# Kernel tuning notes

Measured on AMD Instinct MI355X. Metric: run time of the kernel, lower is better.

The kernel has to match this reference:

```python
import jax, jax.numpy as jnp
import numpy as np

MASK_VALUE = 0.0
LEAKY_SLOPE = 0.2  # tf.keras 'leaky_relu' activation default negative_slope

B, T, F, H, OUT = 256, 512, 256, 1024, 64


def setup_inputs() -> dict:
    key = jax.random.key(0)
    ks = jax.random.split(key, 5)
    x = jax.random.normal(ks[0], (B, T, F), dtype=jnp.float32)
    W = jax.random.normal(ks[1], (F, 4 * H), dtype=jnp.float32) * 0.05
    U = jax.random.normal(ks[2], (H, 4 * H), dtype=jnp.float32) * 0.05
    b = jnp.zeros((4 * H,), dtype=jnp.float32)
    W1 = jax.random.normal(ks[3], (3 * H, H), dtype=jnp.float32) * 0.02
    b1 = jnp.zeros((H,), dtype=jnp.float32)
    W2 = jax.random.normal(ks[4], (H, OUT), dtype=jnp.float32) * 0.02
    b2 = jnp.zeros((OUT,), dtype=jnp.float32)
    return {"x": x, "W": W, "U": U, "b": b, "W1": W1, "b1": b1, "W2": W2, "b2": b2}


def _lstm_final_state(x, mask, W, U, b):
    """Masked LSTM (Keras gate order i,f,g,o); masked steps carry state through.
    Returns final (h, c), each [B, H]. Dropout layers are identity at inference."""
    h0 = jnp.zeros((x.shape[0], H), dtype=x.dtype)
    c0 = jnp.zeros((x.shape[0], H), dtype=x.dtype)
    # Precompute input projection for all timesteps in one big GEMM: [B,T,4H]
    xz = jnp.einsum('btf,fg->btg', x, W) + b

    def step(carry, inp):
        h, c = carry
        xz_t, m_t = inp  # [B,4H], [B]
        z = xz_t + h @ U
        i, f, g, o = jnp.split(z, 4, axis=-1)
        i = jax.nn.sigmoid(i)
        f = jax.nn.sigmoid(f)
        g = jnp.tanh(g)
        o = jax.nn.sigmoid(o)
        c_new = f * c + i * g
        h_new = o * jnp.tanh(c_new)
        m = m_t[:, None]
        h = jnp.where(m, h_new, h)
        c = jnp.where(m, c_new, c)
        return (h, c), None

    xs = (jnp.swapaxes(xz, 0, 1), jnp.swapaxes(mask, 0, 1))  # time-major
    (h, c), _ = jax.lax.scan(step, (h0, c0), xs)
    return h, c


def reference(x, W, U, b, W1, b1, W2, b2):
    mask = jnp.any(x != MASK_VALUE, axis=2)  # [B,T]
    h, c = _lstm_final_state(x, mask, W, U, b)
    # return_state=True with return_sequences=False -> (out, h, c), out == h
    feat = jnp.concatenate([h, h, c], axis=1)  # [B, 3H]
    y = jax.nn.leaky_relu(feat @ W1 + b1, negative_slope=LEAKY_SLOPE)
    return y @ W2 + b2
```

## Files before the change

### kernel.cpp

```cpp
#include <hip/hip_runtime.h>

#define Tt_ 512
#define Ff_ 256
#define Hh_ 1024

typedef unsigned short u16;
typedef unsigned long long u64;
typedef __attribute__((ext_vector_type(8))) short bf16x8;
typedef __attribute__((ext_vector_type(4))) float f32x4;
typedef __attribute__((ext_vector_type(2))) unsigned int u32x2;

#define MFMA(a, b, c) __builtin_amdgcn_mfma_f32_16x16x32_bf16(a, b, c, 0, 0, 0)

__device__ __forceinline__ float bf2f(u16 u){
  union { unsigned int i; float f; } v; v.i = ((unsigned int)u) << 16; return v.f;
}
__device__ __forceinline__ u16 f2bf(float f){
  union { float f; unsigned int i; } v; v.f = f;
  return (u16)((v.i + 0x7FFFu + ((v.i >> 16) & 1u)) >> 16);
}
__device__ __forceinline__ float sigm(float z){ return 1.0f / (1.0f + __expf(-z)); }
__device__ __forceinline__ float tanh_(float z){ return 1.0f - 2.0f / (__expf(2.0f * z) + 1.0f); }
__device__ __forceinline__ float getE(const void* p, size_t i, int isf32){
  return isf32 ? ((const float*)p)[i] : bf2f(((const u16*)p)[i]);
}

template<int SEL>
__device__ __forceinline__ float qb(float v, int lbase){
#if __has_builtin(__builtin_amdgcn_mov_dpp)
  int r = __builtin_amdgcn_mov_dpp(__builtin_bit_cast(int, v), SEL * 0x55, 0xF, 0xF, true);
  return __builtin_bit_cast(float, r);
#else
  return __shfl(v, lbase + SEL, 64);
#endif
}

__global__ void detect_dtype(const u16* __restrict__ p, int* __restrict__ flag){
  int tid = threadIdx.x;
  int plausible = 0;
  for (int i = tid; i < 4096; i += 256){
    u16 u = p[2 * i];
    int ex = (u >> 7) & 0xFF;
    plausible += (((u & 0x7FFF) == 0) || (ex >= 87 && ex <= 133)) ? 1 : 0;
  }
  __shared__ int red[256];
  red[tid] = plausible; __syncthreads();
  for (int s = 128; s > 0; s >>= 1){ if (tid < s) red[tid] += red[tid + s]; __syncthreads(); }
  if (tid == 0) *flag = (red[0] < (4096 * 3) / 5) ? 1 : 0;
}

__global__ void convert_x(const void* __restrict__ x, u16* __restrict__ xb, const int* __restrict__ flags){
  size_t i = ((size_t)blockIdx.x * 256 + threadIdx.x) * 8;
  if (flags[0]){
    const float* xf = (const float*)x + i;
    u16 o[8];
    #pragma unroll
    for (int j = 0; j < 8; ++j) o[j] = f2bf(xf[j]);
    *(bf16x8*)(xb + i) = *(const bf16x8*)o;
  } else {
    *(bf16x8*)(xb + i) = *(const bf16x8*)((const u16*)x + i);
  }
}

__global__ void pack_wu(const void* __restrict__ W, const void* __restrict__ U,
                        const int* __restrict__ flags, u16* __restrict__ WUp){
  int fW = flags[1], fU = flags[2];
  int u = blockIdx.x * 256 + threadIdx.x;
  int nt = u / 10240;
  int rem = u - nt * 10240;
  int kg = rem >> 6, c64 = rem & 63;
  int pc = nt * 64 + c64;
  int g = pc & 3;
  int gb = ((g & 1) << 1) | (g >> 1);
  int oc = gb * 1024 + (pc >> 2);
  u16* dst = WUp + (size_t)u * 8;
  #pragma unroll
  for (int j = 0; j < 8; ++j){
    int k = kg * 8 + j;
    float v = (k < 256) ? getE(W, (size_t)k * 4096 + oc, fW)
                        : getE(U, (size_t)(k - 256) * 4096 + oc, fU);
    dst[j] = f2bf(v);
  }
}

__global__ void pack_w1(const void* __restrict__ W1, const int* __restrict__ flags, u16* __restrict__ W1p){
  int f1 = flags[3];
  int u = blockIdx.x * 256 + threadIdx.x;
  int nt = u >> 14;
  int kg = (u >> 6) & 255, c64 = u & 63;
  int n = nt * 64 + c64;
  u16* dst = W1p + (size_t)u * 8;
  #pragma unroll
  for (int j = 0; j < 8; ++j){
    int k = kg * 8 + j;
    float a = (k < 1024) ? getE(W1, (size_t)k * 1024 + n, f1) : 0.0f;
    a += getE(W1, (size_t)(k + 1024) * 1024 + n, f1);
    dst[j] = f2bf(a);
  }
}

__global__ void pack_w2(const void* __restrict__ W2, const int* __restrict__ flags, u16* __restrict__ W2p){
  int f2 = flags[4];
  int u = blockIdx.x * 256 + threadIdx.x;
  int kg = u >> 6, c64 = u & 63;
  u16* dst = W2p + (size_t)u * 8;
  #pragma unroll
  for (int j = 0; j < 8; ++j) dst[j] = f2bf(getE(W2, (size_t)(kg * 8 + j) * 64 + c64, f2));
}

__global__ void pack_bias(const u16* __restrict__ b, float* __restrict__ br){
  int u = blockIdx.x * 256 + threadIdx.x;
  int g = u & 3;
  int gb = ((g & 1) << 1) | (g >> 1);
  br[u] = bf2f(b[gb * 1024 + (u >> 2)]);
}

__global__ void mask_kernel(const u16* __restrict__ xb, unsigned char* __restrict__ mkT){
  int w = threadIdx.x >> 6, lane = threadIdx.x & 63;
  int row = blockIdx.x * 4 + w;
  u32x2 v = *((const u32x2*)(xb + (size_t)row * 256) + lane);
  int nz = (((v.x & 0x7FFF7FFFu) | (v.y & 0x7FFF7FFFu)) != 0u);
  int a = __any(nz);
  if (lane == 0){
    int b = row >> 9, t = row & 511;
    mkT[(size_t)t * 256 + b] = (unsigned char)(a ? 1 : 0);
  }
}

__launch_bounds__(256, 1)
__global__ void lstm_step(const u16* __restrict__ x, const u16* __restrict__ WUp,
                          const float* __restrict__ br, const unsigned char* __restrict__ mkT,
                          u16* __restrict__ hb0, u16* __restrict__ hb1,
                          u16* __restrict__ cfin, unsigned int* bar){
  __shared__ u64 hsm[8192];
  const int tid = threadIdx.x, bid = blockIdx.x;
  const int lane = tid & 63, w = tid >> 6;
  const int quad = lane >> 4, l15 = lane & 15;
  const int g  = (bid >> 3) & 7;
  const int c  = (bid & 7) | ((bid >> 6) << 3);
  const int r0 = g * 32;
  const int nt = c * 2 + (w >> 1);
  const int bc0 = (w & 1) * 32 + l15;
  const u16* Bb = WUp + (size_t)nt * 81920;
  const int pc0 = c * 128 + w * 32 + l15;
  const float bias0 = br[pc0];
  const float bias1 = br[pc0 + 16];
  const int slot = lane & 3, lbase = lane & 60;
  const int jh0 = pc0 >> 2;
  const int rowE = quad * 4;
  const size_t xrowA = (size_t)(r0 + l15) * (Tt_ * Ff_);
  const size_t xrowB = xrowA + (size_t)16 * Tt_ * Ff_;
  const int swzA = (l15 & 7) << 4;
  char* hb = (char*)hsm;
  unsigned int* mybar = bar + (g << 5);

  f32x4 cst[2][2];
  { f32x4 z4 = {0.f, 0.f, 0.f, 0.f}; cst[0][0] = z4; cst[0][1] = z4; cst[1][0] = z4; cst[1][1] = z4; }

  for (int t = 0; t < Tt_; ++t){
    const u16* hin  = (t & 1) ? hb1 : hb0;
    u16*       hout = (t & 1) ? hb0 : hb1;

    u64 hreg[32];
    #pragma unroll
    for (int i = 0; i < 32; ++i)
      hreg[i] = __hip_atomic_load((const u64*)(hin + (size_t)(r0 + i) * Hh_) + tid,
                                  __ATOMIC_RELAXED, __HIP_MEMORY_SCOPE_AGENT);

    unsigned int mka = *(const unsigned int*)(mkT + (size_t)t * 256 + r0 + rowE);
    unsigned int mkb = *(const unsigned int*)(mkT + (size_t)t * 256 + r0 + rowE + 16);

    f32x4 acc[2][2];
    { f32x4 i0 = {bias0, bias0, bias0, bias0}, i1 = {bias1, bias1, bias1, bias1};
      acc[0][0] = i0; acc[1][0] = i0; acc[0][1] = i1; acc[1][1] = i1; }

    const u16* xp = x + (size_t)t * Ff_;
    #pragma unroll
    for (int ks = 0; ks < 8; ++ks){
      int kq = ks * 32 + quad * 8;
      bf16x8 a0 = *(const bf16x8*)(xp + xrowA + kq);
      bf16x8 a1 = *(const bf16x8*)(xp + xrowB + kq);
      const u16* bp = Bb + (size_t)(ks * 4 + quad) * 512;
      bf16x8 b0 = *(const bf16x8*)(bp + bc0 * 8);
      bf16x8 b1 = *(const bf16x8*)(bp + bc0 * 8 + 128);
      acc[0][0] = MFMA(a0, b0, acc[0][0]);
      acc[0][1] = MFMA(a0, b1, acc[0][1]);
      acc[1][0] = MFMA(a1, b0, acc[1][0]);
      acc[1][1] = MFMA(a1, b1, acc[1][1]);
    }

    {
      int colb = tid * 8;
      #pragma unroll
      for (int i = 0; i < 32; ++i)
        *(u64*)(hb + i * 2048 + (colb ^ ((i & 7) << 4))) = hreg[i];
    }
    __syncthreads();

    #pragma unroll 8
    for (int ks = 0; ks < 32; ++ks){
      int cb = ks * 64 + quad * 16;
      bf16x8 a0 = *(const bf16x8*)(hb + l15 * 2048 + (cb ^ swzA));
      bf16x8 a1 = *(const bf16x8*)(hb + (l15 + 16) * 2048 + (cb ^ swzA));
      const u16* bp = Bb + (size_t)((ks + 8) * 4 + quad) * 512;
      bf16x8 b0 = *(const bf16x8*)(bp + bc0 * 8);
      bf16x8 b1 = *(const bf16x8*)(bp + bc0 * 8 + 128);
      acc[0][0] = MFMA(a0, b0, acc[0][0]);
      acc[0][1] = MFMA(a0, b1, acc[0][1]);
      acc[1][0] = MFMA(a1, b0, acc[1][0]);
      acc[1][1] = MFMA(a1, b1, acc[1][1]);
    }

    #pragma unroll
    for (int mf = 0; mf < 2; ++mf){
      unsigned int mk4 = mf ? mkb : mka;
      #pragma unroll
      for (int nf = 0; nf < 2; ++nf){
        int jh = jh0 + nf * 4;
        #pragma unroll
        for (int reg = 0; reg < 4; ++reg){
          float z = acc[mf][nf][reg];
          float v = (slot == 1) ? tanh_(z) : sigm(z);
          float vi = qb<0>(v, lbase);
          float vg = qb<1>(v, lbase);
          float vf = qb<2>(v, lbase);
          float vo = qb<3>(v, lbase);
          float cv = cst[mf][nf][reg];
          float cn = fmaf(vf, cv, vi * vg);
          float hn = vo * tanh_(cn);
          if (!((mk4 >> (8 * reg)) & 1u)){
            cn = cv;
            int rl = rowE + reg + mf * 16;
            hn = bf2f(*(const u16*)(hb + rl * 2048 + ((jh * 2) ^ ((rl & 7) << 4))));
          }
          cst[mf][nf][reg] = cn;
          if (slot == 0){
            int r = r0 + rowE + reg + mf * 16;
            __hip_atomic_store(&hout[(size_t)r * Hh_ + jh], f2bf(hn),
                               __ATOMIC_RELAXED, __HIP_MEMORY_SCOPE_AGENT);
          }
        }
      }
    }

    __syncthreads();
    if (tid == 0){
      __hip_atomic_fetch_add(mybar, 1u, __ATOMIC_RELAXED, __HIP_MEMORY_SCOPE_AGENT);
      const unsigned int target = (unsigned int)(t + 1) * 32u;
      while (__hip_atomic_load(mybar, __ATOMIC_RELAXED, __HIP_MEMORY_SCOPE_AGENT) < target)
        __builtin_amdgcn_s_sleep(1);
    }
    __syncthreads();
  }

  #pragma unroll
  for (int mf = 0; mf < 2; ++mf)
    #pragma unroll
    for (int nf = 0; nf < 2; ++nf)
      #pragma unroll
      for (int reg = 0; reg < 4; ++reg)
        if (slot == 0){
          int r = r0 + rowE + reg + mf * 16;
          cfin[(size_t)r * Hh_ + jh0 + nf * 4] = f2bf(cst[mf][nf][reg]);
        }
}

__launch_bounds__(256, 1)
__global__ void gemm_head(const u16* __restrict__ A1, const u16* __restrict__ A2,
                          int kSplit, int kSlices, const u16* __restrict__ Bp,
                          int Ntiles, const u16* __restrict__ bias, int act,
                          void* __restrict__ outp, int ldOut, int outF32){
  const int tid = threadIdx.x, bid = blockIdx.x;
  const int lane = tid & 63, w = tid >> 6;
  const int wm = w >> 1, wn = w & 1;
  const int quad = lane >> 4, l15 = lane & 15;
  const int mt = bid / Ntiles, nt = bid - mt * Ntiles;
  const int r0 = mt * 64 + wm * 32 + l15;
  const size_t arow0 = (size_t)r0 * 1024;
  const size_t arow1 = arow0 + (size_t)16 * 1024;
  const int bc0 = wn * 32 + l15;
  const u16* Bb = Bp + (size_t)nt * kSlices * 2048;
  f32x4 acc[2][2];
  { f32x4 z4 = {0.f, 0.f, 0.f, 0.f}; acc[0][0] = z4; acc[0][1] = z4; acc[1][0] = z4; acc[1][1] = z4; }
  #pragma unroll 4
  for (int ks = 0; ks < kSlices; ++ks){
    const u16* ap; int kq;
    if (ks < kSplit){ ap = A1; kq = ks * 32 + quad * 8; }
    else            { ap = A2; kq = (ks - kSplit) * 32 + quad * 8; }
    bf16x8 a0 = *(const bf16x8*)(ap + arow0 + kq);
    bf16x8 a1 = *(const bf16x8*)(ap + arow1 + kq);
    const u16* bp = Bb + (size_t)(ks * 4 + quad) * 512;
    bf16x8 b0 = *(const bf16x8*)(bp + bc0 * 8);
    bf16x8 b1 = *(const bf16x8*)(bp + bc0 * 8 + 128);
    acc[0][0] = MFMA(a0, b0, acc[0][0]);
    acc[0][1] = MFMA(a0, b1, acc[0][1]);
    acc[1][0] = MFMA(a1, b0, acc[1][0]);
    acc[1][1] = MFMA(a1, b1, acc[1][1]);
  }
  #pragma unroll
  for (int mf = 0; mf < 2; ++mf)
    #pragma unroll
    for (int nf = 0; nf < 2; ++nf){
      int cB = nt * 64 + bc0 + nf * 16;
      #pragma unroll
      for (int reg = 0; reg < 4; ++reg){
        int r = mt * 64 + wm * 32 + mf * 16 + quad * 4 + reg;
        float zv = acc[mf][nf][reg] + bf2f(bias[cB]);
        if (act) zv = (zv > 0.f) ? zv : 0.2f * zv;
        if (outF32) ((float*)outp)[(size_t)r * ldOut + cB] = zv;
        else        ((u16*)outp)[(size_t)r * ldOut + cB] = f2bf(zv);
      }
    }
}

extern "C" void kernel_launch(void* const* d_in, const int* in_sizes, int n_in,
                              void* d_out, int out_size, void* d_ws, size_t ws_size,
                              hipStream_t stream){
  const void* x  = d_in[0];
  const void* W  = d_in[1];
  const void* U  = d_in[2];
  const u16*  b  = (const u16*)d_in[3];
  const void* W1 = d_in[4];
  const u16*  b1 = (const u16*)d_in[5];
  const void* W2 = d_in[6];
  const u16*  b2 = (const u16*)d_in[7];
  char* ws = (char*)d_ws;
  size_t o = 0;
  u16* WUp = (u16*)(ws + o);            o += 10485760;
  u16* W1p = (u16*)(ws + o);            o += 4194304;
  u16* W2p = (u16*)(ws + o);            o += 131072;
  float* br = (float*)(ws + o);         o += 16384;
  unsigned char* mk = (unsigned char*)(ws + o); o += 131072;
  u16* hb0 = (u16*)(ws + o);            o += 524288;
  u16* hb1 = (u16*)(ws + o);            o += 524288;
  u16* cfin = (u16*)(ws + o);           o += 524288;
  u16* yb  = (u16*)(ws + o);            o += 524288;
  unsigned int* bar = (unsigned int*)(ws + o); o += 1024;
  int* flg = (int*)(ws + o);            o += 512;
  u16* xb  = (u16*)(ws + o);            o += 67108864;
  if (ws_size < o) return;

  hipMemsetAsync(hb0, 0, 524288, stream);
  hipMemsetAsync(bar, 0, 1024, stream);
  detect_dtype<<<1, 256, 0, stream>>>((const u16*)x,  flg + 0);
  detect_dtype<<<1, 256, 0, stream>>>((const u16*)W,  flg + 1);
  detect_dtype<<<1, 256, 0, stream>>>((const u16*)U,  flg + 2);
  detect_dtype<<<1, 256, 0, stream>>>((const u16*)W1, flg + 3);
  detect_dtype<<<1, 256, 0, stream>>>((const u16*)W2, flg + 4);
  convert_x<<<16384, 256, 0, stream>>>(x, xb, flg);
  pack_wu<<<2560, 256, 0, stream>>>(W, U, flg, WUp);
  pack_w1<<<1024, 256, 0, stream>>>(W1, flg, W1p);
  pack_w2<<<32, 256, 0, stream>>>(W2, flg, W2p);
  pack_bias<<<16, 256, 0, stream>>>(b, br);
  mask_kernel<<<32768, 256, 0, stream>>>(xb, mk);
  lstm_step<<<256, 256, 0, stream>>>(xb, WUp, br, mk, hb0, hb1, cfin, bar);
  gemm_head<<<64, 256, 0, stream>>>(hb0, cfin, 32, 64, W1p, 16, b1, 1, yb, 1024, 0);
  gemm_head<<<4, 256, 0, stream>>>(yb, yb, 32, 32, W2p, 1, b2, 0, d_out, 64, 1);
}
```

Before: 6.179 ms.

## Overlap next-step input projection with barrier wait and split h loading

The x·W input projection for step t+1 is computed between the barrier arrive and the barrier wait, hiding it behind the cross-block synchronisation. The h loads are split into two halves so MFMA work on the first half can start before the second half is in LDS. Part of the recurrent weight slice is cached in shared memory, and h outputs are staged in LDS so each block writes them back with coalesced 64-bit stores. This uses more LDS and adds an extra __syncthreads per step.

```diff
diff --git a/kernel.cpp b/kernel.cpp
--- a/kernel.cpp
+++ b/kernel.cpp
@@ -133,6 +133,8 @@
                           u16* __restrict__ hb0, u16* __restrict__ hb1,
                           u16* __restrict__ cfin, unsigned int* bar){
   __shared__ u64 hsm[8192];
+  __shared__ u16 hstg[1024];
+  __shared__ u16 Bc[2][14336];
   const int tid = threadIdx.x, bid = blockIdx.x;
   const int lane = tid & 63, w = tid >> 6;
   const int quad = lane >> 4, l15 = lane & 15;
@@ -146,35 +148,34 @@
   const float bias0 = br[pc0];
   const float bias1 = br[pc0 + 16];
   const int slot = lane & 3, lbase = lane & 60;
-  const int jh0 = pc0 >> 2;
+  const int jl0 = w * 8 + (l15 >> 2);
   const int rowE = quad * 4;
   const size_t xrowA = (size_t)(r0 + l15) * (Tt_ * Ff_);
   const size_t xrowB = xrowA + (size_t)16 * Tt_ * Ff_;
   const int swzA = (l15 & 7) << 4;
   char* hb = (char*)hsm;
   unsigned int* mybar = bar + (g << 5);
+  const int hr  = tid >> 3;
+  const int hc8 = tid & 7;
+  const size_t hgoff = (size_t)(r0 + hr) * Hh_ + hc8 * 4;
+  const int hldsb = hr * 2048;
+  const int hswz = (hr & 7) << 4;
+  const int hc8b = hc8 * 8;
+
+  for (int i = tid; i < 3584; i += 256){
+    int tile = i / 1792, rem = i - tile * 1792;
+    const u16* src = WUp + (size_t)(c * 2 + tile) * 81920 + 16384 + (size_t)rem * 8;
+    *(bf16x8*)&Bc[tile][rem * 8] = *(const bf16x8*)src;
+  }
 
   f32x4 cst[2][2];
   { f32x4 z4 = {0.f, 0.f, 0.f, 0.f}; cst[0][0] = z4; cst[0][1] = z4; cst[1][0] = z4; cst[1][1] = z4; }
 
-  for (int t = 0; t < Tt_; ++t){
-    const u16* hin  = (t & 1) ? hb1 : hb0;
-    u16*       hout = (t & 1) ? hb0 : hb1;
-
-    u64 hreg[32];
-    #pragma unroll
-    for (int i = 0; i < 32; ++i)
-      hreg[i] = __hip_atomic_load((const u64*)(hin + (size_t)(r0 + i) * Hh_) + tid,
-                                  __ATOMIC_RELAXED, __HIP_MEMORY_SCOPE_AGENT);
-
-    unsigned int mka = *(const unsigned int*)(mkT + (size_t)t * 256 + r0 + rowE);
-    unsigned int mkb = *(const unsigned int*)(mkT + (size_t)t * 256 + r0 + rowE + 16);
-
-    f32x4 acc[2][2];
-    { f32x4 i0 = {bias0, bias0, bias0, bias0}, i1 = {bias1, bias1, bias1, bias1};
-      acc[0][0] = i0; acc[1][0] = i0; acc[0][1] = i1; acc[1][1] = i1; }
-
-    const u16* xp = x + (size_t)t * Ff_;
+  f32x4 accx[2][2];
+  { f32x4 i0 = {bias0, bias0, bias0, bias0}, i1 = {bias1, bias1, bias1, bias1};
+    accx[0][0] = i0; accx[1][0] = i0; accx[0][1] = i1; accx[1][1] = i1; }
+  {
+    const u16* xp = x;
     #pragma unroll
     for (int ks = 0; ks < 8; ++ks){
       int kq = ks * 32 + quad * 8;
@@ -183,22 +184,54 @@
       const u16* bp = Bb + (size_t)(ks * 4 + quad) * 512;
       bf16x8 b0 = *(const bf16x8*)(bp + bc0 * 8);
       bf16x8 b1 = *(const bf16x8*)(bp + bc0 * 8 + 128);
+      accx[0][0] = MFMA(a0, b0, accx[0][0]);
+      accx[0][1] = MFMA(a0, b1, accx[0][1]);
+      accx[1][0] = MFMA(a1, b0, accx[1][0]);
+      accx[1][1] = MFMA(a1, b1, accx[1][1]);
+    }
+  }
+
+  for (int t = 0; t < Tt_; ++t){
+    const u16* hin  = (t & 1) ? hb1 : hb0;
+    u16*       hout = (t & 1) ? hb0 : hb1;
+
+    u64 hA[16], hB[16];
+    #pragma unroll
+    for (int i = 0; i < 16; ++i)
+      hA[i] = __hip_atomic_load((const u64*)(hin + hgoff + i * 32),
+                                __ATOMIC_RELAXED, __HIP_MEMORY_SCOPE_AGENT);
+    #pragma unroll
+    for (int i = 0; i < 16; ++i)
+      hB[i] = __hip_atomic_load((const u64*)(hin + hgoff + (i + 16) * 32),
+                                __ATOMIC_RELAXED, __HIP_MEMORY_SCOPE_AGENT);
+
+    unsigned int mka = *(const unsigned int*)(mkT + (size_t)t * 256 + r0 + rowE);
+    unsigned int mkb = *(const unsigned int*)(mkT + (size_t)t * 256 + r0 + rowE + 16);
+
+    f32x4 acc[2][2];
+    acc[0][0] = accx[0][0]; acc[0][1] = accx[0][1];
+    acc[1][0] = accx[1][0]; acc[1][1] = accx[1][1];
+
+    #pragma unroll
+    for (int i = 0; i < 16; ++i)
+      *(u64*)(hb + hldsb + ((i * 64 + hc8b) ^ hswz)) = hA[i];
+    __syncthreads();
+
+    #pragma unroll
+    for (int ks = 0; ks < 7; ++ks){
+      int cb = ks * 64 + quad * 16;
+      bf16x8 a0 = *(const bf16x8*)(hb + l15 * 2048 + (cb ^ swzA));
+      bf16x8 a1 = *(const bf16x8*)(hb + (l15 + 16) * 2048 + (cb ^ swzA));
+      const u16* bp = &Bc[w >> 1][(ks * 4 + quad) * 512];
+      bf16x8 b0 = *(const bf16x8*)(bp + bc0 * 8);
+      bf16x8 b1 = *(const bf16x8*)(bp + bc0 * 8 + 128);
       acc[0][0] = MFMA(a0, b0, acc[0][0]);
       acc[0][1] = MFMA(a0, b1, acc[0][1]);
       acc[1][0] = MFMA(a1, b0, acc[1][0]);
       acc[1][1] = MFMA(a1, b1, acc[1][1]);
     }
-
-    {
-      int colb = tid * 8;
-      #pragma unroll
-      for (int i = 0; i < 32; ++i)
-        *(u64*)(hb + i * 2048 + (colb ^ ((i & 7) << 4))) = hreg[i];
-    }
-    __syncthreads();
-
-    #pragma unroll 8
-    for (int ks = 0; ks < 32; ++ks){
+    #pragma unroll
+    for (int ks = 7; ks < 16; ++ks){
       int cb = ks * 64 + quad * 16;
       bf16x8 a0 = *(const bf16x8*)(hb + l15 * 2048 + (cb ^ swzA));
       bf16x8 a1 = *(const bf16x8*)(hb + (l15 + 16) * 2048 + (cb ^ swzA));
@@ -212,11 +245,30 @@
     }
 
     #pragma unroll
+    for (int i = 0; i < 16; ++i)
+      *(u64*)(hb + hldsb + (((i + 16) * 64 + hc8b) ^ hswz)) = hB[i];
+    __syncthreads();
+
+    #pragma unroll 8
+    for (int ks = 16; ks < 32; ++ks){
+      int cb = ks * 64 + quad * 16;
+      bf16x8 a0 = *(const bf16x8*)(hb + l15 * 2048 + (cb ^ swzA));
+      bf16x8 a1 = *(const bf16x8*)(hb + (l15 + 16) * 2048 + (cb ^ swzA));
+      const u16* bp = Bb + (size_t)((ks + 8) * 4 + quad) * 512;
+      bf16x8 b0 = *(const bf16x8*)(bp + bc0 * 8);
+      bf16x8 b1 = *(const bf16x8*)(bp + bc0 * 8 + 128);
+      acc[0][0] = MFMA(a0, b0, acc[0][0]);
+      acc[0][1] = MFMA(a0, b1, acc[0][1]);
+      acc[1][0] = MFMA(a1, b0, acc[1][0]);
+      acc[1][1] = MFMA(a1, b1, acc[1][1]);
+    }
+
+    #pragma unroll
     for (int mf = 0; mf < 2; ++mf){
       unsigned int mk4 = mf ? mkb : mka;
       #pragma unroll
       for (int nf = 0; nf < 2; ++nf){
-        int jh = jh0 + nf * 4;
+        int jl = jl0 + nf * 4;
         #pragma unroll
         for (int reg = 0; reg < 4; ++reg){
           float z = acc[mf][nf][reg];
@@ -231,26 +283,56 @@
           if (!((mk4 >> (8 * reg)) & 1u)){
             cn = cv;
             int rl = rowE + reg + mf * 16;
+            int jh = c * 32 + jl;
             hn = bf2f(*(const u16*)(hb + rl * 2048 + ((jh * 2) ^ ((rl & 7) << 4))));
           }
           cst[mf][nf][reg] = cn;
           if (slot == 0){
-            int r = r0 + rowE + reg + mf * 16;
-            __hip_atomic_store(&hout[(size_t)r * Hh_ + jh], f2bf(hn),
-                               __ATOMIC_RELAXED, __HIP_MEMORY_SCOPE_AGENT);
+            int rl = rowE + reg + mf * 16;
+            hstg[rl * 32 + jl] = f2bf(hn);
           }
         }
       }
     }
-
     __syncthreads();
-    if (tid == 0){
-      __hip_atomic_fetch_add(mybar, 1u, __ATOMIC_RELAXED, __HIP_MEMORY_SCOPE_AGENT);
-      const unsigned int target = (unsigned int)(t + 1) * 32u;
-      while (__hip_atomic_load(mybar, __ATOMIC_RELAXED, __HIP_MEMORY_SCOPE_AGENT) < target)
-        __builtin_amdgcn_s_sleep(1);
+
+    {
+      u64 val = ((const u64*)hstg)[tid];
+      __hip_atomic_store((u64*)(hout + (size_t)(r0 + (tid >> 3)) * Hh_ + c * 32 + (tid & 7) * 4),
+                         val, __ATOMIC_RELAXED, __HIP_MEMORY_SCOPE_AGENT);
     }
     __syncthreads();
+
+    if (t < Tt_ - 1){
+      if (tid == 0)
+        __hip_atomic_fetch_add(mybar, 1u, __ATOMIC_RELAXED, __HIP_MEMORY_SCOPE_AGENT);
+
+      { f32x4 i0 = {bias0, bias0, bias0, bias0}, i1 = {bias1, bias1, bias1, bias1};
+        accx[0][0] = i0; accx[1][0] = i0; accx[0][1] = i1; accx[1][1] = i1; }
+      {
+        const u16* xp = x + (size_t)(t + 1) * Ff_;
+        #pragma unroll
+        for (int ks = 0; ks < 8; ++ks){
+          int kq = ks * 32 + quad * 8;
+          bf16x8 a0 = *(const bf16x8*)(xp + xrowA + kq);
+          bf16x8 a1 = *(const bf16x8*)(xp + xrowB + kq);
+          const u16* bp = Bb + (size_t)(ks * 4 + quad) * 512;
+          bf16x8 b0 = *(const bf16x8*)(bp + bc0 * 8);
+          bf16x8 b1 = *(const bf16x8*)(bp + bc0 * 8 + 128);
+          accx[0][0] = MFMA(a0, b0, accx[0][0]);
+          accx[0][1] = MFMA(a0, b1, accx[0][1]);
+          accx[1][0] = MFMA(a1, b0, accx[1][0]);
+          accx[1][1] = MFMA(a1, b1, accx[1][1]);
+        }
+      }
+
+      if (tid == 0){
+        const unsigned int target = (unsigned int)(t + 1) * 32u;
+        while (__hip_atomic_load(mybar, __ATOMIC_RELAXED, __HIP_MEMORY_SCOPE_AGENT) < target)
+          __builtin_amdgcn_s_sleep(1);
+      }
+      __syncthreads();
+    }
   }
 
   #pragma unroll
@@ -261,7 +343,7 @@
       for (int reg = 0; reg < 4; ++reg)
         if (slot == 0){
           int r = r0 + rowE + reg + mf * 16;
-          cfin[(size_t)r * Hh_ + jh0 + nf * 4] = f2bf(cst[mf][nf][reg]);
+          cfin[(size_t)r * Hh_ + c * 32 + jl0 + nf * 4] = f2bf(cst[mf][nf][reg]);
         }
 }
 
```

Result: faster. 5.831 ms (-5.6%).

## Restructure persistent LSTM kernel with 512 threads, LDS weight cache, overlapped input projection

Applied to the files above, without the earlier changes.

Doubles the block to 512 threads, so each wave owns a single 16-column MFMA tile. The input-projection weights and the first slices of U are cached in LDS, and the x-projection for step t+1 is computed while the grid barrier is pending. The h-tile load is split into two halves so the second half's LDS write overlaps the first half's MFMAs. h outputs are staged in LDS and written as coalesced 64-bit stores. The goal is to cut per-step latency on the serial recurrence, at the cost of more LDS and more block-level syncs.

```diff
diff --git a/kernel.cpp b/kernel.cpp
--- a/kernel.cpp
+++ b/kernel.cpp
@@ -127,142 +127,196 @@
   }
 }
 
-__launch_bounds__(256, 1)
+__launch_bounds__(512, 1)
 __global__ void lstm_step(const u16* __restrict__ x, const u16* __restrict__ WUp,
                           const float* __restrict__ br, const unsigned char* __restrict__ mkT,
                           u16* __restrict__ hb0, u16* __restrict__ hb1,
                           u16* __restrict__ cfin, unsigned int* bar){
   __shared__ u64 hsm[8192];
+  __shared__ u16 hstg[1024];
+  __shared__ u16 Bc[2][22528];
   const int tid = threadIdx.x, bid = blockIdx.x;
   const int lane = tid & 63, w = tid >> 6;
   const int quad = lane >> 4, l15 = lane & 15;
   const int g  = (bid >> 3) & 7;
   const int c  = (bid & 7) | ((bid >> 6) << 3);
   const int r0 = g * 32;
-  const int nt = c * 2 + (w >> 1);
-  const int bc0 = (w & 1) * 32 + l15;
+  const int tile = w >> 2;
+  const int nt = c * 2 + tile;
+  const int bc0 = (w & 3) * 16 + l15;
   const u16* Bb = WUp + (size_t)nt * 81920;
-  const int pc0 = c * 128 + w * 32 + l15;
+  const int pc0 = c * 128 + w * 16 + l15;
   const float bias0 = br[pc0];
-  const float bias1 = br[pc0 + 16];
   const int slot = lane & 3, lbase = lane & 60;
-  const int jh0 = pc0 >> 2;
+  const int jl0 = w * 4 + (l15 >> 2);
   const int rowE = quad * 4;
   const size_t xrowA = (size_t)(r0 + l15) * (Tt_ * Ff_);
   const size_t xrowB = xrowA + (size_t)16 * Tt_ * Ff_;
   const int swzA = (l15 & 7) << 4;
   char* hb = (char*)hsm;
   unsigned int* mybar = bar + (g << 5);
-
-  f32x4 cst[2][2];
-  { f32x4 z4 = {0.f, 0.f, 0.f, 0.f}; cst[0][0] = z4; cst[0][1] = z4; cst[1][0] = z4; cst[1][1] = z4; }
-
-  for (int t = 0; t < Tt_; ++t){
-    const u16* hin  = (t & 1) ? hb1 : hb0;
-    u16*       hout = (t & 1) ? hb0 : hb1;
-
-    u64 hreg[32];
-    #pragma unroll
-    for (int i = 0; i < 32; ++i)
-      hreg[i] = __hip_atomic_load((const u64*)(hin + (size_t)(r0 + i) * Hh_) + tid,
-                                  __ATOMIC_RELAXED, __HIP_MEMORY_SCOPE_AGENT);
-
-    unsigned int mka = *(const unsigned int*)(mkT + (size_t)t * 256 + r0 + rowE);
-    unsigned int mkb = *(const unsigned int*)(mkT + (size_t)t * 256 + r0 + rowE + 16);
-
-    f32x4 acc[2][2];
-    { f32x4 i0 = {bias0, bias0, bias0, bias0}, i1 = {bias1, bias1, bias1, bias1};
-      acc[0][0] = i0; acc[1][0] = i0; acc[0][1] = i1; acc[1][1] = i1; }
-
-    const u16* xp = x + (size_t)t * Ff_;
+  const int hr   = tid >> 4;
+  const int hc16 = tid & 15;
+  const size_t hgoff = (size_t)(r0 + hr) * Hh_ + hc16 * 4;
+  const int hldsb = hr * 2048;
+  const int hswz = (hr & 7) << 4;
+  const int hcb = hc16 * 8;
+
+  for (int i = tid; i < 5632; i += 512){
+    int tl = i / 2816, rem = i - tl * 2816;
+    *(bf16x8*)&Bc[tl][rem * 8] =
+      *(const bf16x8*)(WUp + (size_t)(c * 2 + tl) * 81920 + (size_t)rem * 8);
+  }
+  __syncthreads();
+
+  f32x4 cst[2];
+  { f32x4 z4 = {0.f, 0.f, 0.f, 0.f}; cst[0] = z4; cst[1] = z4; }
+
+  f32x4 accx[2];
+  { f32x4 i0 = {bias0, bias0, bias0, bias0}; accx[0] = i0; accx[1] = i0; }
+  {
+    const u16* xp = x;
     #pragma unroll
     for (int ks = 0; ks < 8; ++ks){
       int kq = ks * 32 + quad * 8;
       bf16x8 a0 = *(const bf16x8*)(xp + xrowA + kq);
       bf16x8 a1 = *(const bf16x8*)(xp + xrowB + kq);
-      const u16* bp = Bb + (size_t)(ks * 4 + quad) * 512;
-      bf16x8 b0 = *(const bf16x8*)(bp + bc0 * 8);
-      bf16x8 b1 = *(const bf16x8*)(bp + bc0 * 8 + 128);
-      acc[0][0] = MFMA(a0, b0, acc[0][0]);
-      acc[0][1] = MFMA(a0, b1, acc[0][1]);
-      acc[1][0] = MFMA(a1, b0, acc[1][0]);
-      acc[1][1] = MFMA(a1, b1, acc[1][1]);
-    }
-
-    {
-      int colb = tid * 8;
-      #pragma unroll
-      for (int i = 0; i < 32; ++i)
-        *(u64*)(hb + i * 2048 + (colb ^ ((i & 7) << 4))) = hreg[i];
-    }
+      bf16x8 b0 = *(const bf16x8*)(&Bc[tile][ks * 2048 + quad * 512 + bc0 * 8]);
+      accx[0] = MFMA(a0, b0, accx[0]);
+      accx[1] = MFMA(a1, b0, accx[1]);
+    }
+  }
+
+  for (int t = 0; t < Tt_; ++t){
+    const u16* hin  = (t & 1) ? hb1 : hb0;
+    u16*       hout = (t & 1) ? hb0 : hb1;
+
+    u64 hA[8], hB[8];
+    #pragma unroll
+    for (int i = 0; i < 8; ++i)
+      hA[i] = __hip_atomic_load((const u64*)(hin + hgoff + i * 64),
+                                __ATOMIC_RELAXED, __HIP_MEMORY_SCOPE_AGENT);
+    #pragma unroll
+    for (int i = 0; i < 8; ++i)
+      hB[i] = __hip_atomic_load((const u64*)(hin + hgoff + (i + 8) * 64),
+                                __ATOMIC_RELAXED, __HIP_MEMORY_SCOPE_AGENT);
+
+    unsigned int mka = *(const unsigned int*)(mkT + (size_t)t * 256 + r0 + rowE);
+    unsigned int mkb = *(const unsigned int*)(mkT + (size_t)t * 256 + r0 + rowE + 16);
+
+    f32x4 acc[2];
+    acc[0] = accx[0]; acc[1] = accx[1];
+
+    #pragma unroll
+    for (int i = 0; i < 8; ++i)
+      *(u64*)(hb + hldsb + ((i * 128 + hcb) ^ hswz)) = hA[i];
     __syncthreads();
 
-    #pragma unroll 8
-    for (int ks = 0; ks < 32; ++ks){
+    #pragma unroll
+    for (int ks = 0; ks < 3; ++ks){
       int cb = ks * 64 + quad * 16;
       bf16x8 a0 = *(const bf16x8*)(hb + l15 * 2048 + (cb ^ swzA));
       bf16x8 a1 = *(const bf16x8*)(hb + (l15 + 16) * 2048 + (cb ^ swzA));
-      const u16* bp = Bb + (size_t)((ks + 8) * 4 + quad) * 512;
-      bf16x8 b0 = *(const bf16x8*)(bp + bc0 * 8);
-      bf16x8 b1 = *(const bf16x8*)(bp + bc0 * 8 + 128);
-      acc[0][0] = MFMA(a0, b0, acc[0][0]);
-      acc[0][1] = MFMA(a0, b1, acc[0][1]);
-      acc[1][0] = MFMA(a1, b0, acc[1][0]);
-      acc[1][1] = MFMA(a1, b1, acc[1][1]);
+      bf16x8 b0 = *(const bf16x8*)(&Bc[tile][(ks + 8) * 2048 + quad * 512 + bc0 * 8]);
+      acc[0] = MFMA(a0, b0, acc[0]);
+      acc[1] = MFMA(a1, b0, acc[1]);
+    }
+    #pragma unroll
+    for (int ks = 3; ks < 16; ++ks){
+      int cb = ks * 64 + quad * 16;
+      bf16x8 a0 = *(const bf16x8*)(hb + l15 * 2048 + (cb ^ swzA));
+      bf16x8 a1 = *(const bf16x8*)(hb + (l15 + 16) * 2048 + (cb ^ swzA));
+      bf16x8 b0 = *(const bf16x8*)(Bb + (size_t)((ks + 8) * 4 + quad) * 512 + bc0 * 8);
+      acc[0] = MFMA(a0, b0, acc[0]);
+      acc[1] = MFMA(a1, b0, acc[1]);
+    }
+
+    #pragma unroll
+    for (int i = 0; i < 8; ++i)
+      *(u64*)(hb + hldsb + (((i + 8) * 128 + hcb) ^ hswz)) = hB[i];
+    __syncthreads();
+
+    #pragma unroll
+    for (int ks = 16; ks < 32; ++ks){
+      int cb = ks * 64 + quad * 16;
+      bf16x8 a0 = *(const bf16x8*)(hb + l15 * 2048 + (cb ^ swzA));
+      bf16x8 a1 = *(const bf16x8*)(hb + (l15 + 16) * 2048 + (cb ^ swzA));
+      bf16x8 b0 = *(const bf16x8*)(Bb + (size_t)((ks + 8) * 4 + quad) * 512 + bc0 * 8);
+      acc[0] = MFMA(a0, b0, acc[0]);
+      acc[1] = MFMA(a1, b0, acc[1]);
     }
 
     #pragma unroll
     for (int mf = 0; mf < 2; ++mf){
       unsigned int mk4 = mf ? mkb : mka;
       #pragma unroll
-      for (int nf = 0; nf < 2; ++nf){
-        int jh = jh0 + nf * 4;
-        #pragma unroll
-        for (int reg = 0; reg < 4; ++reg){
-          float z = acc[mf][nf][reg];
-          float v = (slot == 1) ? tanh_(z) : sigm(z);
-          float vi = qb<0>(v, lbase);
-          float vg = qb<1>(v, lbase);
-          float vf = qb<2>(v, lbase);
-          float vo = qb<3>(v, lbase);
-          float cv = cst[mf][nf][reg];
-          float cn = fmaf(vf, cv, vi * vg);
-          float hn = vo * tanh_(cn);
-          if (!((mk4 >> (8 * reg)) & 1u)){
-            cn = cv;
-            int rl = rowE + reg + mf * 16;
-            hn = bf2f(*(const u16*)(hb + rl * 2048 + ((jh * 2) ^ ((rl & 7) << 4))));
-          }
-          cst[mf][nf][reg] = cn;
-          if (slot == 0){
-            int r = r0 + rowE + reg + mf * 16;
-            __hip_atomic_store(&hout[(size_t)r * Hh_ + jh], f2bf(hn),
-                               __ATOMIC_RELAXED, __HIP_MEMORY_SCOPE_AGENT);
-          }
+      for (int reg = 0; reg < 4; ++reg){
+        float z = acc[mf][reg];
+        float v = (slot == 1) ? tanh_(z) : sigm(z);
+        float vi = qb<0>(v, lbase);
+        float vg = qb<1>(v, lbase);
+        float vf = qb<2>(v, lbase);
+        float vo = qb<3>(v, lbase);
+        float cv = cst[mf][reg];
+        float cn = fmaf(vf, cv, vi * vg);
+        float hn = vo * tanh_(cn);
+        if (!((mk4 >> (8 * reg)) & 1u)){
+          cn = cv;
+          int rl = rowE + reg + mf * 16;
+          int jh = c * 32 + jl0;
+          hn = bf2f(*(const u16*)(hb + rl * 2048 + ((jh * 2) ^ ((rl & 7) << 4))));
+        }
+        cst[mf][reg] = cn;
+        if (slot == 0){
+          int rl = rowE + reg + mf * 16;
+          hstg[rl * 32 + jl0] = f2bf(hn);
         }
       }
     }
-
     __syncthreads();
-    if (tid == 0){
-      __hip_atomic_fetch_add(mybar, 1u, __ATOMIC_RELAXED, __HIP_MEMORY_SCOPE_AGENT);
-      const unsigned int target = (unsigned int)(t + 1) * 32u;
-      while (__hip_atomic_load(mybar, __ATOMIC_RELAXED, __HIP_MEMORY_SCOPE_AGENT) < target)
-        __builtin_amdgcn_s_sleep(1);
+
+    if (tid < 256){
+      u64 val = ((const u64*)hstg)[tid];
+      __hip_atomic_store((u64*)(hout + (size_t)(r0 + (tid >> 3)) * Hh_ + c * 32 + (tid & 7) * 4),
+                         val, __ATOMIC_RELAXED, __HIP_MEMORY_SCOPE_AGENT);
     }
     __syncthreads();
+
+    if (t < Tt_ - 1){
+      if (tid == 0)
+        __hip_atomic_fetch_add(mybar, 1u, __ATOMIC_RELAXED, __HIP_MEMORY_SCOPE_AGENT);
+
+      { f32x4 i0 = {bias0, bias0, bias0, bias0}; accx[0] = i0; accx[1] = i0; }
+      {
+        const u16* xp = x + (size_t)(t + 1) * Ff_;
+        #pragma unroll
+        for (int ks = 0; ks < 8; ++ks){
+          int kq = ks * 32 + quad * 8;
+          bf16x8 a0 = *(const bf16x8*)(xp + xrowA + kq);
+          bf16x8 a1 = *(const bf16x8*)(xp + xrowB + kq);
+          bf16x8 b0 = *(const bf16x8*)(&Bc[tile][ks * 2048 + quad * 512 + bc0 * 8]);
+          accx[0] = MFMA(a0, b0, accx[0]);
+          accx[1] = MFMA(a1, b0, accx[1]);
+        }
+      }
+
+      if (tid == 0){
+        const unsigned int target = (unsigned int)(t + 1) * 32u;
+        while (__hip_atomic_load(mybar, __ATOMIC_RELAXED, __HIP_MEMORY_SCOPE_AGENT) < target)
+          __builtin_amdgcn_s_sleep(1);
+      }
+      __syncthreads();
+    }
   }
 
   #pragma unroll
   for (int mf = 0; mf < 2; ++mf)
     #pragma unroll
-    for (int nf = 0; nf < 2; ++nf)
-      #pragma unroll
-      for (int reg = 0; reg < 4; ++reg)
-        if (slot == 0){
-          int r = r0 + rowE + reg + mf * 16;
-          cfin[(size_t)r * Hh_ + jh0 + nf * 4] = f2bf(cst[mf][nf][reg]);
-        }
+    for (int reg = 0; reg < 4; ++reg)
+      if (slot == 0){
+        int r = r0 + rowE + reg + mf * 16;
+        cfin[(size_t)r * Hh_ + c * 32 + jl0] = f2bf(cst[mf][reg]);
+      }
 }
 
 __launch_bounds__(256, 1)
@@ -353,7 +407,7 @@
   pack_w2<<<32, 256, 0, stream>>>(W2, flg, W2p);
   pack_bias<<<16, 256, 0, stream>>>(b, br);
   mask_kernel<<<32768, 256, 0, stream>>>(xb, mk);
-  lstm_step<<<256, 256, 0, stream>>>(xb, WUp, br, mk, hb0, hb1, cfin, bar);
+  lstm_step<<<256, 512, 0, stream>>>(xb, WUp, br, mk, hb0, hb1, cfin, bar);
   gemm_head<<<64, 256, 0, stream>>>(hb0, cfin, 32, 64, W1p, 16, b1, 1, yb, 1024, 0);
   gemm_head<<<4, 256, 0, stream>>>(yb, yb, 32, 32, W2p, 1, b2, 0, d_out, 64, 1);
 }
```

Measured after the change: 4.946 ms (median of 2 runs). 19.9% less time.

## Split LSTM step K-dimension across two wave groups with LDS reduction

Applied to the files above, without the earlier changes.

Doubles the block to 512 threads, with two halves each handling half of the K dimension of the x and h projections. Partial accumulators are exchanged through shared memory so each half finishes the gate math for 16 of the 32 rows. The x-projection weights are cached in LDS once for all timesteps. New h values are staged in LDS and written out as coalesced 64-bit atomic stores. The final grid barrier is skipped. This aims to cut per-step latency on the serial recurrence, at the cost of extra LDS traffic and two more __syncthreads per step.

```diff
diff --git a/kernel.cpp b/kernel.cpp
--- a/kernel.cpp
+++ b/kernel.cpp
@@ -5,6 +5,7 @@
 #define Hh_ 1024
 
 typedef unsigned short u16;
+typedef unsigned int u32;
 typedef unsigned long long u64;
 typedef __attribute__((ext_vector_type(8))) short bf16x8;
 typedef __attribute__((ext_vector_type(4))) float f32x4;
@@ -127,60 +128,103 @@
   }
 }
 
-__launch_bounds__(256, 1)
+__launch_bounds__(512, 2)
 __global__ void lstm_step(const u16* __restrict__ x, const u16* __restrict__ WUp,
                           const float* __restrict__ br, const unsigned char* __restrict__ mkT,
                           u16* __restrict__ hb0, u16* __restrict__ hb1,
                           u16* __restrict__ cfin, unsigned int* bar){
   __shared__ u64 hsm[8192];
+  __shared__ u16 hstg[1024];
+  __shared__ u16 Bc[2][16384];
+  __shared__ f32x4 red[2][4][64][2];
   const int tid = threadIdx.x, bid = blockIdx.x;
   const int lane = tid & 63, w = tid >> 6;
   const int quad = lane >> 4, l15 = lane & 15;
   const int g  = (bid >> 3) & 7;
   const int c  = (bid & 7) | ((bid >> 6) << 3);
   const int r0 = g * 32;
-  const int nt = c * 2 + (w >> 1);
-  const int bc0 = (w & 1) * 32 + l15;
-  const u16* Bb = WUp + (size_t)nt * 81920;
-  const int pc0 = c * 128 + w * 32 + l15;
+  const int kh = w >> 2;
+  const int cs = w & 3;
+  const int tile = cs >> 1;
+  const int bc0 = (cs & 1) * 32 + l15;
+  const u16* Bb = WUp + (size_t)(c * 2 + tile) * 81920;
+  const int pc0 = c * 128 + cs * 32 + l15;
   const float bias0 = br[pc0];
   const float bias1 = br[pc0 + 16];
   const int slot = lane & 3, lbase = lane & 60;
-  const int jh0 = pc0 >> 2;
+  const int jl0 = cs * 8 + (l15 >> 2);
+  const int rowW = kh * 16;
   const int rowE = quad * 4;
   const size_t xrowA = (size_t)(r0 + l15) * (Tt_ * Ff_);
   const size_t xrowB = xrowA + (size_t)16 * Tt_ * Ff_;
   const int swzA = (l15 & 7) << 4;
   char* hb = (char*)hsm;
   unsigned int* mybar = bar + (g << 5);
-
-  f32x4 cst[2][2];
-  { f32x4 z4 = {0.f, 0.f, 0.f, 0.f}; cst[0][0] = z4; cst[0][1] = z4; cst[1][0] = z4; cst[1][1] = z4; }
+  const int hr   = tid >> 4;
+  const int hc16 = tid & 15;
+  const size_t hgoff = (size_t)(r0 + hr) * Hh_ + hc16 * 4;
+  const int hldsb = hr * 2048;
+  const int hswz = (hr & 7) << 4;
+  const int hcb = hc16 * 8;
+
+  for (int i = tid; i < 4096; i += 512){
+    int tl = i >> 11, rem = i & 2047;
+    *(bf16x8*)&Bc[tl][rem * 8] =
+      *(const bf16x8*)(WUp + (size_t)(c * 2 + tl) * 81920 + (size_t)rem * 8);
+  }
+  __syncthreads();
+
+  f32x4 cst0 = {0.f, 0.f, 0.f, 0.f};
+  f32x4 cst1 = {0.f, 0.f, 0.f, 0.f};
 
   for (int t = 0; t < Tt_; ++t){
     const u16* hin  = (t & 1) ? hb1 : hb0;
     u16*       hout = (t & 1) ? hb0 : hb1;
 
-    u64 hreg[32];
-    #pragma unroll
-    for (int i = 0; i < 32; ++i)
-      hreg[i] = __hip_atomic_load((const u64*)(hin + (size_t)(r0 + i) * Hh_) + tid,
-                                  __ATOMIC_RELAXED, __HIP_MEMORY_SCOPE_AGENT);
-
-    unsigned int mka = *(const unsigned int*)(mkT + (size_t)t * 256 + r0 + rowE);
-    unsigned int mkb = *(const unsigned int*)(mkT + (size_t)t * 256 + r0 + rowE + 16);
+    const u16* xp = x + (size_t)t * Ff_;
+    bf16x8 xa[4][2];
+    #pragma unroll
+    for (int ks = 0; ks < 4; ++ks){
+      int kq = (kh * 4 + ks) * 32 + quad * 8;
+      xa[ks][0] = *(const bf16x8*)(xp + xrowA + kq);
+      xa[ks][1] = *(const bf16x8*)(xp + xrowB + kq);
+    }
+    u64 hl[16];
+    #pragma unroll
+    for (int i = 0; i < 16; ++i)
+      hl[i] = __hip_atomic_load((const u64*)(hin + hgoff + i * 64),
+                                __ATOMIC_RELAXED, __HIP_MEMORY_SCOPE_AGENT);
+
+    unsigned int mk4 = *(const u32*)(mkT + (size_t)t * 256 + r0 + rowW + rowE);
 
     f32x4 acc[2][2];
-    { f32x4 i0 = {bias0, bias0, bias0, bias0}, i1 = {bias1, bias1, bias1, bias1};
+    { f32x4 z4 = {0.f, 0.f, 0.f, 0.f};
+      f32x4 i0 = kh ? z4 : (f32x4){bias0, bias0, bias0, bias0};
+      f32x4 i1 = kh ? z4 : (f32x4){bias1, bias1, bias1, bias1};
       acc[0][0] = i0; acc[1][0] = i0; acc[0][1] = i1; acc[1][1] = i1; }
-
-    const u16* xp = x + (size_t)t * Ff_;
-    #pragma unroll
-    for (int ks = 0; ks < 8; ++ks){
-      int kq = ks * 32 + quad * 8;
-      bf16x8 a0 = *(const bf16x8*)(xp + xrowA + kq);
-      bf16x8 a1 = *(const bf16x8*)(xp + xrowB + kq);
-      const u16* bp = Bb + (size_t)(ks * 4 + quad) * 512;
+    #pragma unroll
+    for (int ks = 0; ks < 4; ++ks){
+      const u16* bp = &Bc[tile][((kh * 4 + ks) * 4 + quad) * 512 + bc0 * 8];
+      bf16x8 b0 = *(const bf16x8*)(bp);
+      bf16x8 b1 = *(const bf16x8*)(bp + 128);
+      acc[0][0] = MFMA(xa[ks][0], b0, acc[0][0]);
+      acc[0][1] = MFMA(xa[ks][0], b1, acc[0][1]);
+      acc[1][0] = MFMA(xa[ks][1], b0, acc[1][0]);
+      acc[1][1] = MFMA(xa[ks][1], b1, acc[1][1]);
+    }
+
+    #pragma unroll
+    for (int i = 0; i < 16; ++i)
+      *(u64*)(hb + hldsb + ((i * 128 + hcb) ^ hswz)) = hl[i];
+    __syncthreads();
+
+    #pragma unroll
+    for (int ks = 0; ks < 16; ++ks){
+      int s = kh * 16 + ks;
+      int cb = s * 64 + quad * 16;
+      bf16x8 a0 = *(const bf16x8*)(hb + l15 * 2048 + (cb ^ swzA));
+      bf16x8 a1 = *(const bf16x8*)(hb + (l15 + 16) * 2048 + (cb ^ swzA));
+      const u16* bp = Bb + (size_t)((s + 8) * 4 + quad) * 512;
       bf16x8 b0 = *(const bf16x8*)(bp + bc0 * 8);
       bf16x8 b1 = *(const bf16x8*)(bp + bc0 * 8 + 128);
       acc[0][0] = MFMA(a0, b0, acc[0][0]);
@@ -189,80 +233,67 @@
       acc[1][1] = MFMA(a1, b1, acc[1][1]);
     }
 
-    {
-      int colb = tid * 8;
+    red[kh][cs][lane][0] = acc[kh ^ 1][0];
+    red[kh][cs][lane][1] = acc[kh ^ 1][1];
+    __syncthreads();
+    f32x4 accK0 = acc[kh][0] + red[kh ^ 1][cs][lane][0];
+    f32x4 accK1 = acc[kh][1] + red[kh ^ 1][cs][lane][1];
+
+    #pragma unroll
+    for (int nf = 0; nf < 2; ++nf){
+      int jl = jl0 + nf * 4;
       #pragma unroll
-      for (int i = 0; i < 32; ++i)
-        *(u64*)(hb + i * 2048 + (colb ^ ((i & 7) << 4))) = hreg[i];
-    }
-    __syncthreads();
-
-    #pragma unroll 8
-    for (int ks = 0; ks < 32; ++ks){
-      int cb = ks * 64 + quad * 16;
-      bf16x8 a0 = *(const bf16x8*)(hb + l15 * 2048 + (cb ^ swzA));
-      bf16x8 a1 = *(const bf16x8*)(hb + (l15 + 16) * 2048 + (cb ^ swzA));
-      const u16* bp = Bb + (size_t)((ks + 8) * 4 + quad) * 512;
-      bf16x8 b0 = *(const bf16x8*)(bp + bc0 * 8);
-      bf16x8 b1 = *(const bf16x8*)(bp + bc0 * 8 + 128);
-      acc[0][0] = MFMA(a0, b0, acc[0][0]);
-      acc[0][1] = MFMA(a0, b1, acc[0][1]);
-      acc[1][0] = MFMA(a1, b0, acc[1][0]);
-      acc[1][1] = MFMA(a1, b1, acc[1][1]);
-    }
-
-    #pragma unroll
-    for (int mf = 0; mf < 2; ++mf){
-      unsigned int mk4 = mf ? mkb : mka;
-      #pragma unroll
-      for (int nf = 0; nf < 2; ++nf){
-        int jh = jh0 + nf * 4;
-        #pragma unroll
-        for (int reg = 0; reg < 4; ++reg){
-          float z = acc[mf][nf][reg];
-          float v = (slot == 1) ? tanh_(z) : sigm(z);
-          float vi = qb<0>(v, lbase);
-          float vg = qb<1>(v, lbase);
-          float vf = qb<2>(v, lbase);
-          float vo = qb<3>(v, lbase);
-          float cv = cst[mf][nf][reg];
-          float cn = fmaf(vf, cv, vi * vg);
-          float hn = vo * tanh_(cn);
-          if (!((mk4 >> (8 * reg)) & 1u)){
-            cn = cv;
-            int rl = rowE + reg + mf * 16;
-            hn = bf2f(*(const u16*)(hb + rl * 2048 + ((jh * 2) ^ ((rl & 7) << 4))));
-          }
-          cst[mf][nf][reg] = cn;
-          if (slot == 0){
-            int r = r0 + rowE + reg + mf * 16;
-            __hip_atomic_store(&hout[(size_t)r * Hh_ + jh], f2bf(hn),
-                               __ATOMIC_RELAXED, __HIP_MEMORY_SCOPE_AGENT);
-          }
+      for (int reg = 0; reg < 4; ++reg){
+        float z = nf ? accK1[reg] : accK0[reg];
+        float v = (slot == 1) ? tanh_(z) : sigm(z);
+        float vi = qb<0>(v, lbase);
+        float vg = qb<1>(v, lbase);
+        float vf = qb<2>(v, lbase);
+        float vo = qb<3>(v, lbase);
+        float cv = nf ? cst1[reg] : cst0[reg];
+        float cn = fmaf(vf, cv, vi * vg);
+        float hn = vo * tanh_(cn);
+        if (!((mk4 >> (8 * reg)) & 1u)){
+          cn = cv;
+          int rl = rowW + rowE + reg;
+          int jh = c * 32 + jl;
+          hn = bf2f(*(const u16*)(hb + rl * 2048 + ((jh * 2) ^ ((rl & 7) << 4))));
+        }
+        if (nf) cst1[reg] = cn; else cst0[reg] = cn;
+        if (slot == 0){
+          int rl = rowW + rowE + reg;
+          hstg[rl * 32 + jl] = f2bf(hn);
         }
       }
     }
-
     __syncthreads();
-    if (tid == 0){
-      __hip_atomic_fetch_add(mybar, 1u, __ATOMIC_RELAXED, __HIP_MEMORY_SCOPE_AGENT);
-      const unsigned int target = (unsigned int)(t + 1) * 32u;
-      while (__hip_atomic_load(mybar, __ATOMIC_RELAXED, __HIP_MEMORY_SCOPE_AGENT) < target)
-        __builtin_amdgcn_s_sleep(1);
+
+    if (tid < 256){
+      u64 val = ((const u64*)hstg)[tid];
+      __hip_atomic_store((u64*)(hout + (size_t)(r0 + (tid >> 3)) * Hh_ + c * 32 + (tid & 7) * 4),
+                         val, __ATOMIC_RELAXED, __HIP_MEMORY_SCOPE_AGENT);
     }
     __syncthreads();
-  }
-
-  #pragma unroll
-  for (int mf = 0; mf < 2; ++mf)
-    #pragma unroll
-    for (int nf = 0; nf < 2; ++nf)
-      #pragma unroll
-      for (int reg = 0; reg < 4; ++reg)
-        if (slot == 0){
-          int r = r0 + rowE + reg + mf * 16;
-          cfin[(size_t)r * Hh_ + jh0 + nf * 4] = f2bf(cst[mf][nf][reg]);
-        }
+
+    if (t < Tt_ - 1){
+      if (tid == 0){
+        __hip_atomic_fetch_add(mybar, 1u, __ATOMIC_RELAXED, __HIP_MEMORY_SCOPE_AGENT);
+        const unsigned int target = (unsigned int)(t + 1) * 32u;
+        while (__hip_atomic_load(mybar, __ATOMIC_RELAXED, __HIP_MEMORY_SCOPE_AGENT) < target)
+          __builtin_amdgcn_s_sleep(1);
+      }
+      __syncthreads();
+    }
+  }
+
+  #pragma unroll
+  for (int nf = 0; nf < 2; ++nf)
+    #pragma unroll
+    for (int reg = 0; reg < 4; ++reg)
+      if (slot == 0){
+        int r = r0 + rowW + rowE + reg;
+        cfin[(size_t)r * Hh_ + c * 32 + jl0 + nf * 4] = f2bf(nf ? cst1[reg] : cst0[reg]);
+      }
 }
 
 __launch_bounds__(256, 1)
@@ -353,7 +384,7 @@
   pack_w2<<<32, 256, 0, stream>>>(W2, flg, W2p);
   pack_bias<<<16, 256, 0, stream>>>(b, br);
   mask_kernel<<<32768, 256, 0, stream>>>(xb, mk);
-  lstm_step<<<256, 256, 0, stream>>>(xb, WUp, br, mk, hb0, hb1, cfin, bar);
+  lstm_step<<<256, 512, 0, stream>>>(xb, WUp, br, mk, hb0, hb1, cfin, bar);
   gemm_head<<<64, 256, 0, stream>>>(hb0, cfin, 32, 64, W1p, 16, b1, 1, yb, 1024, 0);
   gemm_head<<<4, 256, 0, stream>>>(yb, yb, 32, 32, W2p, 1, b2, 0, d_out, 64, 1);
 }
```

After: 6.707 ms. +8.5%, slower.
